# Kernel tuning notes

Measured on AMD Instinct MI355X. Metric: run time of the kernel, lower is better.

## Reference

```python
import jax, jax.numpy as jnp
import numpy as np

C = 512

def _xavier(key, shape, gain=1.0):
    fan_in, fan_out = shape[1], shape[0]
    a = gain * np.sqrt(6.0 / (fan_in + fan_out))
    return jax.random.uniform(key, shape, jnp.float32, -a, a)

def setup_inputs() -> dict:
    key = jax.random.key(0)
    ks = jax.random.split(key, 5)
    x = jax.random.normal(ks[0], (32, C, 32, 32), jnp.float32)
    # 1x1 conv weights as [out_ch, in_ch]; biases zero-init per module
    Wq = _xavier(ks[1], (C, C))
    Wk = _xavier(ks[2], (C, C))
    Wv = _xavier(ks[3], (C, C))
    Wo = _xavier(ks[4], (C, C), gain=1e-05)
    zeros = jnp.zeros((C,), jnp.float32)
    return {"x": x, "Wq": Wq, "bq": zeros, "Wk": Wk, "bk": zeros,
            "Wv": Wv, "bv": zeros, "Wo": Wo, "bo": zeros}

def _proj(x, W, b):
    # 1x1 conv: x [B,C,H,W], W [Cout,Cin] -> [B,Cout,H,W]
    return jnp.einsum('bchw,oc->bohw', x, W) + b[None, :, None, None]

def reference(x, Wq, bq, Wk, bk, Wv, bv, Wo, bo):
    B, Cc, H, W = x.shape
    q = _proj(x, Wq, bq).transpose(0, 2, 3, 1).reshape(B, H * W, Cc)  # [B,HW,C]
    k = _proj(x, Wk, bk).reshape(B, Cc, H * W)                        # [B,C,HW]
    v = _proj(x, Wv, bv).transpose(0, 2, 3, 1).reshape(B, H * W, Cc)  # [B,HW,C]
    w = jnp.einsum('bnc,bcm->bnm', q, k) * (Cc ** -0.5)               # [B,HW,HW]
    w = jax.nn.softmax(w, axis=-1)
    h = jnp.einsum('bnm,bmc->bnc', w, v)                              # [B,HW,C]
    h = h.reshape(B, H, W, Cc).transpose(0, 3, 1, 2)                  # [B,C,H,W]
    h = _proj(h, Wo, bo)
    return x + h
```

## Files before the change

### kernel.cpp

```cpp
#include <hip/hip_runtime.h>
#include <stdint.h>


#define CD 512
#define NSP 1024
#define SCALE_EXP2 0.06376339f
#define WO_SCALE 4194304.0f
#define WO_INV   2.384185791015625e-7f

using bf16x8 = __attribute__((ext_vector_type(8))) short;
using f32x4  = __attribute__((ext_vector_type(4))) float;
typedef long i64v;

__device__ __forceinline__ unsigned char f2f8(float f) {
    unsigned int r;
    asm("v_cvt_pk_fp8_f32 %0, %1, %1" : "=v"(r) : "v"(f));
    return (unsigned char)(r & 0xffu);
}
__device__ __forceinline__ unsigned int f4_to_f8x4(float a, float b, float c, float d) {
    unsigned int r = 0;
    asm("v_cvt_pk_fp8_f32 %0, %2, %3\n\t"
        "v_cvt_pk_fp8_f32 %0, %4, %5 op_sel:[0,0,1]"
        : "=v"(r) : "0"(r), "v"(a), "v"(b), "v"(c), "v"(d));
    return r;
}
__device__ __forceinline__ void gl_lds16(const void* g, void* l) {
    __builtin_amdgcn_global_load_lds(
        (const __attribute__((address_space(1))) void*)g,
        (__attribute__((address_space(3))) void*)l, 16, 0, 0);
}

__global__ __launch_bounds__(256) void cvt_all(
    const float* __restrict__ Wq, const float* __restrict__ Wk,
    const float* __restrict__ Wv, const float* __restrict__ Wo,
    const float* __restrict__ bq, const float* __restrict__ bk,
    unsigned char* __restrict__ w8, float* __restrict__ bqk)
{
    int idx = blockIdx.x * 256 + threadIdx.x;
    int which = idx >> 18, off = idx & 262143;
    const float* src = which == 0 ? Wq : which == 1 ? Wk : which == 2 ? Wv : Wo;
    float v = src[off] * (which == 3 ? WO_SCALE : 1.0f);
    w8[idx] = f2f8(v);
    if (idx < 1024) bqk[idx] = (idx < 512) ? bq[idx] : bk[idx - 512];
}

__global__ __launch_bounds__(256) void transpose_x(const float* __restrict__ x,
                                                   unsigned char* __restrict__ xt) {
    __shared__ float t[32][33];
    int b = blockIdx.z;
    int n0 = blockIdx.x * 32, c0 = blockIdx.y * 32;
    const float* xb = x + (size_t)b * CD * NSP;
    unsigned char* xtb = xt + (size_t)b * NSP * CD;
    int tx = threadIdx.x, ty = threadIdx.y;
    #pragma unroll
    for (int i = 0; i < 4; ++i)
        t[ty + i * 8][tx] = xb[(size_t)(c0 + ty + i * 8) * NSP + n0 + tx];
    __syncthreads();
    #pragma unroll
    for (int i = 0; i < 4; ++i)
        xtb[(size_t)(n0 + ty + i * 8) * CD + c0 + tx] = f2f8(t[tx][ty + i * 8]);
}

template<int BIAS_MODE, bool RESID, bool OUT_F32>
__global__ __launch_bounds__(256)
void gemm_bt8(const unsigned char* __restrict__ A,
              const unsigned char* __restrict__ B,
              void* __restrict__ Cv,
              const float* __restrict__ bias,
              const float* __restrict__ resid,
              int K, int lda, int ldb, int ldc,
              long sA, long sB, long sC, long sR, float alpha)
{
    __shared__ __align__(16) unsigned char As[2][128 * 64];
    __shared__ __align__(16) unsigned char Bs[2][128 * 64];

    const int z = blockIdx.z;
    const unsigned char* Ab = A + (size_t)z * sA + (size_t)blockIdx.y * 128 * lda;
    const unsigned char* Bb = B + (size_t)z * sB + (size_t)blockIdx.x * 128 * ldb;

    const int t = threadIdx.x;
    const int lane = t & 63;
    const int wave = t >> 6;
    const int wr = wave >> 1, wc = wave & 1;
    const int lr = lane & 15, lk = lane >> 4;

    f32x4 acc[4][4] = {};

    const int KT = K >> 6;
    auto stage = [&](int kt, int buf) {
        int k0 = kt << 6;
        #pragma unroll
        for (int i = 0; i < 2; ++i) {
            int rb = i * 64 + wave * 16;
            int row = rb + (lane >> 2);
            int src = (lane & 3) ^ ((row >> 1) & 3);
            gl_lds16(Ab + (size_t)row * lda + k0 + src * 16, &As[buf][rb * 64]);
            gl_lds16(Bb + (size_t)row * ldb + k0 + src * 16, &Bs[buf][rb * 64]);
        }
    };
    stage(0, 0);
    for (int kt = 0; kt < KT; ++kt) {
        int cur = kt & 1;
        if (kt + 1 < KT) {
            stage(kt + 1, cur ^ 1);
            asm volatile("s_waitcnt vmcnt(4)" ::: "memory");
        } else {
            asm volatile("s_waitcnt vmcnt(0)" ::: "memory");
        }
        __builtin_amdgcn_s_barrier();
        const unsigned char* Ac = &As[cur][0];
        const unsigned char* Bc = &Bs[cur][0];
        #pragma unroll
        for (int kk = 0; kk < 2; ++kk) {
            int c16 = kk * 2 + (lk >> 1);
            int half = (lk & 1) * 8;
            i64v af[4], bfr[4];
            #pragma unroll
            for (int f = 0; f < 4; ++f) {
                int arow = wr * 64 + f * 16 + lr;
                af[f] = *(const i64v*)&Ac[arow * 64 + ((c16 ^ ((arow >> 1) & 3)) << 4) + half];
                int brow = wc * 64 + f * 16 + lr;
                bfr[f] = *(const i64v*)&Bc[brow * 64 + ((c16 ^ ((brow >> 1) & 3)) << 4) + half];
            }
            #pragma unroll
            for (int fm = 0; fm < 4; ++fm)
                #pragma unroll
                for (int fn = 0; fn < 4; ++fn)
                    acc[fm][fn] = __builtin_amdgcn_mfma_f32_16x16x32_fp8_fp8(
                        af[fm], bfr[fn], acc[fm][fn], 0, 0, 0);
        }
        asm volatile("s_waitcnt lgkmcnt(0)" ::: "memory");
        __builtin_amdgcn_s_barrier();
    }

    const int m0 = blockIdx.y * 128;
    const int n0 = blockIdx.x * 128;
    unsigned char* C8 = (unsigned char*)Cv + (size_t)z * sC;
    float* Cf = (float*)Cv + (size_t)z * sC;
    const float* rp = RESID ? resid + (size_t)z * sR : nullptr;
    #pragma unroll
    for (int fm = 0; fm < 4; ++fm) {
        #pragma unroll
        for (int fn = 0; fn < 4; ++fn) {
            int col = n0 + wc * 64 + fn * 16 + lr;
            int rowb = m0 + wr * 64 + fm * 16 + lk * 4;
            #pragma unroll
            for (int j = 0; j < 4; ++j) {
                int row = rowb + j;
                float v = acc[fm][fn][j] * alpha;
                if (BIAS_MODE == 1) v += bias[col];
                if (BIAS_MODE == 2) v += bias[row];
                if (RESID) v += rp[(size_t)row * ldc + col];
                if (OUT_F32) Cf[(size_t)row * ldc + col] = v;
                else         C8[(size_t)row * ldc + col] = f2f8(v);
            }
        }
    }
}

__global__ __launch_bounds__(256, 2)
void flash_attn(const unsigned char* __restrict__ Q,
                const unsigned char* __restrict__ Kg,
                const unsigned char* __restrict__ Vg,
                unsigned char* __restrict__ H)
{
    __shared__ __align__(16) unsigned char Ks[2][32 * 512];
    __shared__ __align__(16) unsigned char Vs[2][512 * 32];
    __shared__ __align__(16) unsigned char Ps[64 * 40];
    __shared__ __align__(16) float Ls[64];
    __shared__ int flag;

    const int p = blockIdx.x;
    const int b  = (p & 7) + 8 * (p >> 7);
    const int qt = (p >> 3) & 15;

    const int tid = threadIdx.x;
    const int w = tid >> 6, lane = tid & 63;
    const int lr = lane & 15, lk = lane >> 4;
    const int q0 = qt * 64 + w * 16;

    i64v qf[16];
    const unsigned char* qp = Q + ((size_t)b * NSP + q0 + lr) * 1024 + lk * 8;
    #pragma unroll
    for (int st = 0; st < 16; ++st) qf[st] = *(const i64v*)(qp + st * 32);

    f32x4 o[4][8] = {};
    float m = -3.0e38f, l = 0.f;

    const unsigned char* Kb = Kg + (size_t)b * NSP * 1024;
    const unsigned char* Vb = Vg + (size_t)b * CD * 1024;

    auto stageK = [&](int t, int buf) {
        int kv0 = t * 32;
        #pragma unroll
        for (int i = 0; i < 4; ++i) {
            int rb = w * 8 + i * 2;
            int row = rb + (lane >> 5);
            int src = (lane & 31) ^ (row & 7);
            gl_lds16(Kb + (size_t)(kv0 + row) * 1024 + src * 16, &Ks[buf][rb * 512]);
        }
    };
    auto stageV = [&](int t, int buf) {
        int kv0 = t * 32;
        #pragma unroll
        for (int i = 0; i < 4; ++i) {
            int cb = w * 128 + i * 32;
            int c = cb + (lane >> 1);
            int srch = (lane & 1) ^ (c & 1);
            gl_lds16(Vb + (size_t)c * 1024 + kv0 + srch * 16, &Vs[buf][cb * 32]);
        }
    };

    if (tid == 0) flag = -1;
    stageK(0, 0); stageV(0, 0);
    asm volatile("s_waitcnt vmcnt(0) lgkmcnt(0)" ::: "memory");
    __builtin_amdgcn_s_barrier();

    for (int t = 0; t < 32; ++t) {
        const int cur = t & 1;
        if (t < 31) { stageK(t + 1, cur ^ 1); stageV(t + 1, cur ^ 1); }

        f32x4 s[2] = {};
        const unsigned char* Kc = &Ks[cur][0];
        __builtin_amdgcn_s_setprio(1);
        #pragma unroll
        for (int st = 0; st < 16; ++st) {
            int c16 = st * 2 + (lk >> 1);
            int half = (lk & 1) * 8;
            #pragma unroll
            for (int kvf = 0; kvf < 2; ++kvf) {
                int row = kvf * 16 + lr;
                i64v kf = *(const i64v*)&Kc[row * 512 + ((c16 ^ (row & 7)) << 4) + half];
                s[kvf] = __builtin_amdgcn_mfma_f32_16x16x32_fp8_fp8(kf, qf[st], s[kvf], 0, 0, 0);
            }
        }
        __builtin_amdgcn_s_setprio(0);

        #pragma unroll
        for (int kvf = 0; kvf < 2; ++kvf)
            #pragma unroll
            for (int j = 0; j < 4; ++j) s[kvf][j] *= SCALE_EXP2;

        float pm = fmaxf(fmaxf(fmaxf(s[0][0], s[0][1]), fmaxf(s[0][2], s[0][3])),
                         fmaxf(fmaxf(s[1][0], s[1][1]), fmaxf(s[1][2], s[1][3])));
        pm = fmaxf(pm, __shfl_xor(pm, 16));
        pm = fmaxf(pm, __shfl_xor(pm, 32));
        bool ev = !__all(pm - m <= 8.0f);
        float mn = fmaxf(m, pm);
        float sc = ev ? exp2f(m - mn) : 1.0f;
        if (ev) { m = mn; l *= sc; }
        if (lk == 0) Ls[w * 16 + lr] = sc;
        if (ev && lane == 0) flag = t;

        float rs = 0.f;
        #pragma unroll
        for (int kvf = 0; kvf < 2; ++kvf)
            #pragma unroll
            for (int j = 0; j < 4; ++j) {
                s[kvf][j] = exp2f(s[kvf][j] - m);
                rs += s[kvf][j];
            }
        rs += __shfl_xor(rs, 16);
        rs += __shfl_xor(rs, 32);
        l += rs;

        #pragma unroll
        for (int kvf = 0; kvf < 2; ++kvf) {
            unsigned int pk = f4_to_f8x4(s[kvf][0], s[kvf][1], s[kvf][2], s[kvf][3]);
            *(unsigned int*)&Ps[(w * 16 + lr) * 40 + kvf * 16 + lk * 4] = pk;
        }
        asm volatile("s_waitcnt lgkmcnt(0)" ::: "memory");
        __builtin_amdgcn_s_barrier();

        if (flag == t) {
            #pragma unroll
            for (int qf2 = 0; qf2 < 4; ++qf2) {
                f32x4 scv = *(const f32x4*)&Ls[qf2 * 16 + lk * 4];
                #pragma unroll
                for (int cf = 0; cf < 8; ++cf) {
                    o[qf2][cf][0] *= scv[0]; o[qf2][cf][1] *= scv[1];
                    o[qf2][cf][2] *= scv[2]; o[qf2][cf][3] *= scv[3];
                }
            }
        }
        const unsigned char* Vc = &Vs[cur][0];
        i64v vfr[8];
        #pragma unroll
        for (int cf = 0; cf < 8; ++cf) {
            int c = w * 128 + cf * 16 + lr;
            vfr[cf] = *(const i64v*)&Vc[c * 32 + (((lk >> 1) ^ (c & 1)) << 4) + (lk & 1) * 8];
        }
        __builtin_amdgcn_s_setprio(1);
        #pragma unroll
        for (int qf2 = 0; qf2 < 4; ++qf2) {
            i64v pa = *(const i64v*)&Ps[(qf2 * 16 + lr) * 40 + lk * 8];
            #pragma unroll
            for (int cf = 0; cf < 8; ++cf)
                o[qf2][cf] = __builtin_amdgcn_mfma_f32_16x16x32_fp8_fp8(
                    pa, vfr[cf], o[qf2][cf], 0, 0, 0);
        }
        __builtin_amdgcn_s_setprio(0);
        asm volatile("s_waitcnt vmcnt(0) lgkmcnt(0)" ::: "memory");
        __builtin_amdgcn_s_barrier();
    }

    if (lk == 0) Ls[w * 16 + lr] = 1.0f / l;
    asm volatile("s_waitcnt lgkmcnt(0)" ::: "memory");
    __builtin_amdgcn_s_barrier();
    unsigned char* Hp = H + ((size_t)b * NSP + qt * 64) * CD + w * 128;
    #pragma unroll
    for (int qf2 = 0; qf2 < 4; ++qf2) {
        f32x4 li = *(const f32x4*)&Ls[qf2 * 16 + lk * 4];
        #pragma unroll
        for (int cf = 0; cf < 8; ++cf) {
            #pragma unroll
            for (int j = 0; j < 4; ++j)
                Hp[(size_t)(qf2 * 16 + lk * 4 + j) * CD + cf * 16 + lr] =
                    f2f8(o[qf2][cf][j] * li[j]);
        }
    }
}

extern "C" void kernel_launch(void* const* d_in, const int* in_sizes, int n_in,
                              void* d_out, int out_size, void* d_ws, size_t ws_size,
                              hipStream_t stream)
{
    const float* x  = (const float*)d_in[0];
    const float* Wq = (const float*)d_in[1];
    const float* bq = (const float*)d_in[2];
    const float* Wk = (const float*)d_in[3];
    const float* bk = (const float*)d_in[4];
    const float* Wv = (const float*)d_in[5];
    const float* bv = (const float*)d_in[6];
    const float* Wo = (const float*)d_in[7];
    const float* bo = (const float*)d_in[8];
    float* out = (float*)d_out;

    unsigned char* w = (unsigned char*)d_ws;
    unsigned char* W8  = w;
    float*         bqk = (float*)(w + 1048576);
    unsigned char* Xt8 = w + 1052672;
    unsigned char* QK8 = w + 17829888;
    unsigned char* Vc8 = w + 51384320;
    unsigned char* H8  = w + 68161536;

    cvt_all<<<4096, 256, 0, stream>>>(Wq, Wk, Wv, Wo, bq, bk, W8, bqk);
    transpose_x<<<dim3(32, 16, 32), dim3(32, 8), 0, stream>>>(x, Xt8);

    gemm_bt8<1, false, false><<<dim3(8, 256, 1), 256, 0, stream>>>(
        Xt8, W8, QK8, bqk, nullptr, 512, 512, 512, 1024, 0, 0, 0, 0, 1.0f);

    gemm_bt8<2, false, false><<<dim3(8, 4, 32), 256, 0, stream>>>(
        W8 + 524288, Xt8, Vc8, bv, nullptr, 512, 512, 512, 1024,
        0, 524288, 524288, 0, 1.0f);

    flash_attn<<<512, 256, 0, stream>>>(QK8, QK8 + 512, Vc8, H8);

    gemm_bt8<2, true, true><<<dim3(8, 4, 32), 256, 0, stream>>>(
        W8 + 786432, H8, out, bo, x, 512, 512, 512, 1024,
        0, 524288, 524288, 524288, WO_INV);
}
```

Measured before the change: 211.4 us.

## Restructure flash attention: 128-query blocks, 64-wide KV tiles, software-pipelined QK/PV

The attention kernel now uses 8 waves per block covering 128 queries, doubles the KV tile to 64, and double-buffers the P and scale buffers. The QK^T and softmax for the next tile are issued after the PV MMAs of the current tile, and K is prefetched two tiles ahead, which removes one barrier per iteration and overlaps the two phases. Shared memory use rises to about 150KB and the grid is halved to 256 blocks, which may limit occupancy and wave-level parallelism.

```diff
diff --git a/kernel.cpp b/kernel.cpp
--- a/kernel.cpp
+++ b/kernel.cpp
@@ -158,103 +158,97 @@
     }
 }
 
-__global__ __launch_bounds__(256, 2)
+__global__ __launch_bounds__(512, 2)
 void flash_attn(const unsigned char* __restrict__ Q,
                 const unsigned char* __restrict__ Kg,
                 const unsigned char* __restrict__ Vg,
                 unsigned char* __restrict__ H)
 {
-    __shared__ __align__(16) unsigned char Ks[2][32 * 512];
-    __shared__ __align__(16) unsigned char Vs[2][512 * 32];
-    __shared__ __align__(16) unsigned char Ps[64 * 40];
-    __shared__ __align__(16) float Ls[64];
-    __shared__ int flag;
+    __shared__ __align__(16) unsigned char Ks[2][64 * 512];
+    __shared__ __align__(16) unsigned char Vs[2][512 * 64];
+    __shared__ __align__(16) unsigned char Ps[2][128 * 72];
+    __shared__ __align__(16) float Ls[2][128];
+    __shared__ int flags[2];
 
     const int p = blockIdx.x;
-    const int b  = (p & 7) + 8 * (p >> 7);
-    const int qt = (p >> 3) & 15;
+    const int b  = ((p >> 6) << 3) + (p & 7);
+    const int qt = (p >> 3) & 7;
 
     const int tid = threadIdx.x;
     const int w = tid >> 6, lane = tid & 63;
     const int lr = lane & 15, lk = lane >> 4;
-    const int q0 = qt * 64 + w * 16;
+    const int q0 = qt * 128 + w * 16;
 
     i64v qf[16];
     const unsigned char* qp = Q + ((size_t)b * NSP + q0 + lr) * 1024 + lk * 8;
     #pragma unroll
     for (int st = 0; st < 16; ++st) qf[st] = *(const i64v*)(qp + st * 32);
 
-    f32x4 o[4][8] = {};
+    f32x4 o[8][4] = {};
     float m = -3.0e38f, l = 0.f;
 
     const unsigned char* Kb = Kg + (size_t)b * NSP * 1024;
     const unsigned char* Vb = Vg + (size_t)b * CD * 1024;
 
     auto stageK = [&](int t, int buf) {
-        int kv0 = t * 32;
+        int kv0 = t * 64;
         #pragma unroll
         for (int i = 0; i < 4; ++i) {
-            int rb = w * 8 + i * 2;
+            int rb = i * 16 + w * 2;
             int row = rb + (lane >> 5);
             int src = (lane & 31) ^ (row & 7);
             gl_lds16(Kb + (size_t)(kv0 + row) * 1024 + src * 16, &Ks[buf][rb * 512]);
         }
     };
     auto stageV = [&](int t, int buf) {
-        int kv0 = t * 32;
+        int kv0 = t * 64;
         #pragma unroll
         for (int i = 0; i < 4; ++i) {
-            int cb = w * 128 + i * 32;
-            int c = cb + (lane >> 1);
-            int srch = (lane & 1) ^ (c & 1);
-            gl_lds16(Vb + (size_t)c * 1024 + kv0 + srch * 16, &Vs[buf][cb * 32]);
+            int cb = i * 128 + w * 16;
+            int c = cb + (lane >> 2);
+            int src = (lane & 3) ^ ((c >> 1) & 3);
+            gl_lds16(Vb + (size_t)c * 1024 + kv0 + src * 16, &Vs[buf][cb * 64]);
         }
     };
 
-    if (tid == 0) flag = -1;
-    stageK(0, 0); stageV(0, 0);
-    asm volatile("s_waitcnt vmcnt(0) lgkmcnt(0)" ::: "memory");
-    __builtin_amdgcn_s_barrier();
-
-    for (int t = 0; t < 32; ++t) {
-        const int cur = t & 1;
-        if (t < 31) { stageK(t + 1, cur ^ 1); stageV(t + 1, cur ^ 1); }
-
-        f32x4 s[2] = {};
-        const unsigned char* Kc = &Ks[cur][0];
+    auto qksm = [&](int tau) {
+        const int pb = tau & 1;
+        const unsigned char* Kc = &Ks[pb][0];
+        f32x4 s[4] = {};
         __builtin_amdgcn_s_setprio(1);
         #pragma unroll
         for (int st = 0; st < 16; ++st) {
             int c16 = st * 2 + (lk >> 1);
             int half = (lk & 1) * 8;
             #pragma unroll
-            for (int kvf = 0; kvf < 2; ++kvf) {
+            for (int kvf = 0; kvf < 4; ++kvf) {
                 int row = kvf * 16 + lr;
                 i64v kf = *(const i64v*)&Kc[row * 512 + ((c16 ^ (row & 7)) << 4) + half];
                 s[kvf] = __builtin_amdgcn_mfma_f32_16x16x32_fp8_fp8(kf, qf[st], s[kvf], 0, 0, 0);
             }
         }
         __builtin_amdgcn_s_setprio(0);
-
-        #pragma unroll
-        for (int kvf = 0; kvf < 2; ++kvf)
+        #pragma unroll
+        for (int kvf = 0; kvf < 4; ++kvf)
             #pragma unroll
             for (int j = 0; j < 4; ++j) s[kvf][j] *= SCALE_EXP2;
 
         float pm = fmaxf(fmaxf(fmaxf(s[0][0], s[0][1]), fmaxf(s[0][2], s[0][3])),
                          fmaxf(fmaxf(s[1][0], s[1][1]), fmaxf(s[1][2], s[1][3])));
+        pm = fmaxf(pm, fmaxf(fmaxf(fmaxf(s[2][0], s[2][1]), fmaxf(s[2][2], s[2][3])),
+                             fmaxf(fmaxf(s[3][0], s[3][1]), fmaxf(s[3][2], s[3][3]))));
         pm = fmaxf(pm, __shfl_xor(pm, 16));
         pm = fmaxf(pm, __shfl_xor(pm, 32));
         bool ev = !__all(pm - m <= 8.0f);
         float mn = fmaxf(m, pm);
         float sc = ev ? exp2f(m - mn) : 1.0f;
         if (ev) { m = mn; l *= sc; }
-        if (lk == 0) Ls[w * 16 + lr] = sc;
-        if (ev && lane == 0) flag = t;
+        if (lk == 0) Ls[pb][w * 16 + lr] = sc;
+        if (ev && lane == 0) flags[pb] = tau;
 
         float rs = 0.f;
         #pragma unroll
-        for (int kvf = 0; kvf < 2; ++kvf)
+        for (int kvf = 0; kvf < 4; ++kvf)
             #pragma unroll
             for (int j = 0; j < 4; ++j) {
                 s[kvf][j] = exp2f(s[kvf][j] - m);
@@ -265,54 +259,75 @@
         l += rs;
 
         #pragma unroll
-        for (int kvf = 0; kvf < 2; ++kvf) {
+        for (int kvf = 0; kvf < 4; ++kvf) {
             unsigned int pk = f4_to_f8x4(s[kvf][0], s[kvf][1], s[kvf][2], s[kvf][3]);
-            *(unsigned int*)&Ps[(w * 16 + lr) * 40 + kvf * 16 + lk * 4] = pk;
-        }
-        asm volatile("s_waitcnt lgkmcnt(0)" ::: "memory");
-        __builtin_amdgcn_s_barrier();
-
-        if (flag == t) {
-            #pragma unroll
-            for (int qf2 = 0; qf2 < 4; ++qf2) {
-                f32x4 scv = *(const f32x4*)&Ls[qf2 * 16 + lk * 4];
+            *(unsigned int*)&Ps[pb][(w * 16 + lr) * 72 + kvf * 16 + lk * 4] = pk;
+        }
+    };
+
+    if (tid == 0) { flags[0] = -1; flags[1] = -1; }
+    stageK(0, 0); stageV(0, 0);
+    asm volatile("s_waitcnt vmcnt(0) lgkmcnt(0)" ::: "memory");
+    __builtin_amdgcn_s_barrier();
+    stageK(1, 1);
+    qksm(0);
+    asm volatile("s_waitcnt vmcnt(0) lgkmcnt(0)" ::: "memory");
+    __builtin_amdgcn_s_barrier();
+
+    for (int t = 0; t < 16; ++t) {
+        const int cur = t & 1;
+        if (t < 14) stageK(t + 2, cur);
+        if (t < 15) stageV(t + 1, cur ^ 1);
+
+        if (flags[cur] == t) {
+            #pragma unroll
+            for (int qf2 = 0; qf2 < 8; ++qf2) {
+                f32x4 scv = *(const f32x4*)&Ls[cur][qf2 * 16 + lk * 4];
                 #pragma unroll
-                for (int cf = 0; cf < 8; ++cf) {
+                for (int cf = 0; cf < 4; ++cf) {
                     o[qf2][cf][0] *= scv[0]; o[qf2][cf][1] *= scv[1];
                     o[qf2][cf][2] *= scv[2]; o[qf2][cf][3] *= scv[3];
                 }
             }
         }
         const unsigned char* Vc = &Vs[cur][0];
-        i64v vfr[8];
-        #pragma unroll
-        for (int cf = 0; cf < 8; ++cf) {
-            int c = w * 128 + cf * 16 + lr;
-            vfr[cf] = *(const i64v*)&Vc[c * 32 + (((lk >> 1) ^ (c & 1)) << 4) + (lk & 1) * 8];
-        }
         __builtin_amdgcn_s_setprio(1);
         #pragma unroll
-        for (int qf2 = 0; qf2 < 4; ++qf2) {
-            i64v pa = *(const i64v*)&Ps[(qf2 * 16 + lr) * 40 + lk * 8];
-            #pragma unroll
-            for (int cf = 0; cf < 8; ++cf)
-                o[qf2][cf] = __builtin_amdgcn_mfma_f32_16x16x32_fp8_fp8(
-                    pa, vfr[cf], o[qf2][cf], 0, 0, 0);
+        for (int ks = 0; ks < 2; ++ks) {
+            int c16 = ks * 2 + (lk >> 1);
+            int half = (lk & 1) * 8;
+            i64v vfr[4];
+            #pragma unroll
+            for (int cf = 0; cf < 4; ++cf) {
+                int c = w * 64 + cf * 16 + lr;
+                vfr[cf] = *(const i64v*)&Vc[c * 64 + ((c16 ^ ((c >> 1) & 3)) << 4) + half];
+            }
+            #pragma unroll
+            for (int qf2 = 0; qf2 < 8; ++qf2) {
+                i64v pa = *(const i64v*)&Ps[cur][(qf2 * 16 + lr) * 72 + ks * 32 + lk * 8];
+                #pragma unroll
+                for (int cf = 0; cf < 4; ++cf)
+                    o[qf2][cf] = __builtin_amdgcn_mfma_f32_16x16x32_fp8_fp8(
+                        pa, vfr[cf], o[qf2][cf], 0, 0, 0);
+            }
         }
         __builtin_amdgcn_s_setprio(0);
+
+        if (t < 15) qksm(t + 1);
+
         asm volatile("s_waitcnt vmcnt(0) lgkmcnt(0)" ::: "memory");
         __builtin_amdgcn_s_barrier();
     }
 
-    if (lk == 0) Ls[w * 16 + lr] = 1.0f / l;
+    if (lk == 0) Ls[0][w * 16 + lr] = 1.0f / l;
     asm volatile("s_waitcnt lgkmcnt(0)" ::: "memory");
     __builtin_amdgcn_s_barrier();
-    unsigned char* Hp = H + ((size_t)b * NSP + qt * 64) * CD + w * 128;
-    #pragma unroll
-    for (int qf2 = 0; qf2 < 4; ++qf2) {
-        f32x4 li = *(const f32x4*)&Ls[qf2 * 16 + lk * 4];
-        #pragma unroll
-        for (int cf = 0; cf < 8; ++cf) {
+    unsigned char* Hp = H + ((size_t)b * NSP + qt * 128) * CD + w * 64;
+    #pragma unroll
+    for (int qf2 = 0; qf2 < 8; ++qf2) {
+        f32x4 li = *(const f32x4*)&Ls[0][qf2 * 16 + lk * 4];
+        #pragma unroll
+        for (int cf = 0; cf < 4; ++cf) {
             #pragma unroll
             for (int j = 0; j < 4; ++j)
                 Hp[(size_t)(qf2 * 16 + lk * 4 + j) * CD + cf * 16 + lr] =
@@ -354,7 +369,7 @@
         W8 + 524288, Xt8, Vc8, bv, nullptr, 512, 512, 512, 1024,
         0, 524288, 524288, 0, 1.0f);
 
-    flash_attn<<<512, 256, 0, stream>>>(QK8, QK8 + 512, Vc8, H8);
+    flash_attn<<<256, 512, 0, stream>>>(QK8, QK8 + 512, Vc8, H8);
 
     gemm_bt8<2, true, true><<<dim3(8, 4, 32), 256, 0, stream>>>(
         W8 + 786432, H8, out, bo, x, 512, 512, 512, 1024,
```

Result: faster. 196.9 us (-6.8%).
